# Kernel optimization log

Hardware: AMD Instinct MI355X
Metric: run time of the kernel (lower is better)

## Reference

```python
import jax, jax.numpy as jnp
import numpy as np

OBS = 256      # observation_space_size == state_vector_len
SV = 2047      # STATE_VECTORS = WMG_MAX_OBS
D = 256        # tfm_vec_size = 8 heads * 32 head_size
H = 8
HD = 32
L = 2          # TFM_NUM_LAYERS
FF = 1024      # TFM_HIDDEN_SIZE
ACH = 512      # AC_HIDDEN_LAYER_SIZE
A = 16         # action_space_size


def setup_inputs() -> dict:
    key = jax.random.key(0)
    ks = jax.random.split(key, 24)
    r = lambda k, s: (jax.random.normal(k, s, jnp.float32) * 0.02)
    inp = {
        "observation": jax.random.normal(ks[0], (OBS,), jnp.float32),
        "old_vectors": jax.random.normal(ks[1], (SV, OBS), jnp.float32),
        "W_core": r(ks[2], (OBS, D)), "b_core": jnp.zeros((D,), jnp.float32),
        # memo embedding takes cat(state_vec, age_onehot) of size OBS+SV
        "W_memo": r(ks[3], (OBS + SV, D)), "b_memo": jnp.zeros((D,), jnp.float32),
        "Wq": r(ks[4], (L, D, D)), "bq": jnp.zeros((L, D), jnp.float32),
        "Wk": r(ks[5], (L, D, D)), "bk": jnp.zeros((L, D), jnp.float32),
        "Wv": r(ks[6], (L, D, D)), "bv": jnp.zeros((L, D), jnp.float32),
        "Wo": r(ks[7], (L, D, D)), "bo": jnp.zeros((L, D), jnp.float32),
        "ln1_g": jnp.ones((L, D), jnp.float32), "ln1_b": jnp.zeros((L, D), jnp.float32),
        "ln2_g": jnp.ones((L, D), jnp.float32), "ln2_b": jnp.zeros((L, D), jnp.float32),
        "W_ff1": r(ks[8], (L, D, FF)), "b_ff1": jnp.zeros((L, FF), jnp.float32),
        "W_ff2": r(ks[9], (L, FF, D)), "b_ff2": jnp.zeros((L, D), jnp.float32),
        "aW1": r(ks[10], (D, ACH)), "ab1": jnp.zeros((ACH,), jnp.float32),
        "aW2": r(ks[11], (ACH, ACH)), "ab2": jnp.zeros((ACH,), jnp.float32),
        "aWo": r(ks[12], (ACH, A)), "abo": jnp.zeros((A,), jnp.float32),
        "cW1": r(ks[13], (D, ACH)), "cb1": jnp.zeros((ACH,), jnp.float32),
        "cW2": r(ks[14], (ACH, ACH)), "cb2": jnp.zeros((ACH,), jnp.float32),
        "cWo": r(ks[15], (ACH, 1)), "cbo": jnp.zeros((1,), jnp.float32),
    }
    return inp


def _ln(x, g, b, eps=1e-5):
    m = jnp.mean(x, axis=-1, keepdims=True)
    v = jnp.mean(jnp.square(x - m), axis=-1, keepdims=True)
    return (x - m) * jax.lax.rsqrt(v + eps) * g + b


def reference(observation, old_vectors, W_core, b_core, W_memo, b_memo,
              Wq, bq, Wk, bk, Wv, bv, Wo, bo,
              ln1_g, ln1_b, ln2_g, ln2_b, W_ff1, b_ff1, W_ff2, b_ff2,
              aW1, ab1, aW2, ab2, aWo, abo, cW1, cb1, cW2, cb2, cWo, cbo):
    # core embedding [D]
    emb0 = observation @ W_core + b_core
    # fused memo + age-onehot embedding: cat(vec_i, e_i) @ W_memo == vec_i @ W_memo[:OBS] + W_memo[OBS+i]
    memo_emb = old_vectors @ W_memo[:OBS] + W_memo[OBS:] + b_memo  # [SV, D]
    x = jnp.concatenate([emb0[None, :], memo_emb], axis=0)[None]   # [1, 1+SV, D]
    S = 1 + SV
    scale = 1.0 / np.sqrt(HD).astype(np.float32)
    for l in range(L):
        q = (x @ Wq[l] + bq[l]).reshape(1, S, H, HD)
        k = (x @ Wk[l] + bk[l]).reshape(1, S, H, HD)
        v = (x @ Wv[l] + bv[l]).reshape(1, S, H, HD)
        scores = jnp.einsum('bqhd,bkhd->bhqk', q, k) * scale       # [1,H,S,S]
        probs = jax.nn.softmax(scores, axis=-1)
        ctx = jnp.einsum('bhqk,bkhd->bqhd', probs, v).reshape(1, S, D)
        x = _ln(x + ctx @ Wo[l] + bo[l], ln1_g[l], ln1_b[l])
        h = jax.nn.gelu(x @ W_ff1[l] + b_ff1[l])
        x = _ln(x + h @ W_ff2[l] + b_ff2[l], ln2_g[l], ln2_b[l])
    t = x[:, 0, :]                                                 # [1, D]
    ha = jnp.tanh(jnp.tanh(t @ aW1 + ab1) @ aW2 + ab2)
    policy = ha @ aWo + abo                                        # [1, A] logits
    hc = jnp.tanh(jnp.tanh(t @ cW1 + cb1) @ cW2 + cb2)
    value_est = hc @ cWo + cbo                                     # [1, 1]
    # WMG_MAX_MEMOS == 0 path: new state vector is tanh(observation)
    new_vector = jnp.tanh(observation)                             # [OBS]
    return value_est, policy, new_vector
```

## Files before the change

### kernel.cpp

```cpp
#include <hip/hip_runtime.h>
#include <stdint.h>

typedef __attribute__((ext_vector_type(8))) short bf16x8;
typedef __attribute__((ext_vector_type(4))) float f32x4;

constexpr int kSEQ = 2048;
constexpr int kD   = 256;
constexpr int kHD  = 32;
constexpr int kFF  = 1024;
constexpr int kA   = 16;

__device__ __forceinline__ unsigned short f2b(float f) {
  union { float f; unsigned int u; } v; v.f = f;
  unsigned int r = v.u + 0x7FFFu + ((v.u >> 16) & 1u);
  return (unsigned short)(r >> 16);
}

struct ConvTable {
  const float* src[13];
  int K[13];
  int N[13];
  int dst[13];
  int tstart[14];
};

union SharedU {
  struct { unsigned short lt[64][72]; } cv;
  struct { unsigned short Al[64][40]; unsigned short Bl[32][40]; } g64;
  struct { unsigned short Kl[64][40]; unsigned short Vt[32][72];
           unsigned short Pl[4][16][72]; } at;
};

struct MegaParams {
  ConvTable tab;
  const float *obs, *oldv, *Wcore, *bcore, *Wmemo0, *bmemo, *Wmemo2;
  const float *bq, *bk, *bv, *bo, *ln1g, *ln1b, *ln2g, *ln2b, *bff1, *bff2;
  const float *aW1, *ab1, *aW2, *ab2, *aWo, *abo;
  const float *cW1, *cb1, *cW2, *cb2, *cWo, *cbo;
  float* xf; unsigned short* xb;
  unsigned short *qb, *kb, *vb, *wT;
  float *pacc, *pml, *h1, *h2, *out;
  int oQKV[2], oWoT[2], oFF1[2], oFF2[2];
  int convJobs, nsplit, tpb;
};

__device__ void conv_job(const MegaParams& p, SharedU& sh, int job) {
  const int tid = threadIdx.x;
  if (job == p.convJobs) {
    float a = p.bcore[tid];
    #pragma unroll 8
    for (int k = 0; k < 256; k++) a += p.obs[k] * p.Wcore[k * kD + tid];
    p.xf[tid] = a;
    p.xb[tid] = f2b(a);
    return;
  }
  int m = 0;
  while (job >= p.tab.tstart[m + 1]) m++;
  const int tloc = job - p.tab.tstart[m];
  const int N = p.tab.N[m], K = p.tab.K[m];
  const int ntile = N >> 6;
  const int k0 = (tloc / ntile) * 64, n0 = (tloc % ntile) * 64;
  const float* src = p.tab.src[m];
  {
    const int r = tid >> 2, c16 = (tid & 3) * 16;
    const float* sp = src + (size_t)(k0 + r) * N + n0 + c16;
    #pragma unroll
    for (int j = 0; j < 16; j++) sh.cv.lt[r][c16 + j] = f2b(sp[j]);
  }
  __syncthreads();
  {
    const int n = tid >> 2, kc = (tid & 3) * 16;
    unsigned short* dp = p.wT + p.tab.dst[m] + (size_t)(n0 + n) * K + k0 + kc;
    unsigned short g[16];
    #pragma unroll
    for (int j = 0; j < 16; j++) g[j] = sh.cv.lt[kc + j][n];
    *(bf16x8*)dp = *(bf16x8*)&g[0];
    *(bf16x8*)(dp + 8) = *(bf16x8*)&g[8];
  }
}

__device__ void memo_job(const MegaParams& p, SharedU& sh, int job) {
  const int tid = threadIdx.x;
  const int w = tid >> 6, l = tid & 63, lg = l >> 4, lr = l & 15;
  const int sr = tid >> 2, sk = (tid & 3) * 8;
  const int kr = tid >> 3, nc = (tid & 7) * 4;
  const int m0 = (job & 31) * 64, n0 = (job >> 5) * 32;
  f32x4 acc[2];
  #pragma unroll
  for (int c = 0; c < 2; c++)
    #pragma unroll
    for (int i = 0; i < 4; i++) acc[c][i] = 0.f;

  auto loadA = [&](int k0) -> bf16x8 {
    bf16x8 av;
    if (m0 + sr < 2047) {
      const float* ap = p.oldv + (size_t)(m0 + sr) * 256 + k0 + sk;
      #pragma unroll
      for (int j = 0; j < 8; j++) av[j] = (short)f2b(ap[j]);
    } else {
      #pragma unroll
      for (int j = 0; j < 8; j++) av[j] = 0;
    }
    return av;
  };
  auto loadB = [&](int k0, float* b4) {
    const float* bp = p.Wmemo0 + (size_t)(k0 + kr) * kD + n0 + nc;
    #pragma unroll
    for (int j = 0; j < 4; j++) b4[j] = bp[j];
  };

  bf16x8 av = loadA(0);
  float b4[4];
  loadB(0, b4);

  for (int k0 = 0; k0 < 256; k0 += 32) {
    __syncthreads();
    *(bf16x8*)&sh.g64.Al[sr][sk] = av;
    #pragma unroll
    for (int j = 0; j < 4; j++) sh.g64.Bl[nc + j][kr] = f2b(b4[j]);
    __syncthreads();
    if (k0 + 32 < 256) {
      av = loadA(k0 + 32);
      loadB(k0 + 32, b4);
    }
    bf16x8 af = *(bf16x8*)&sh.g64.Al[w * 16 + lr][8 * lg];
    #pragma unroll
    for (int c = 0; c < 2; c++) {
      bf16x8 bf = *(bf16x8*)&sh.g64.Bl[c * 16 + lr][8 * lg];
      acc[c] = __builtin_amdgcn_mfma_f32_16x16x32_bf16(af, bf, acc[c], 0, 0, 0);
    }
  }

  #pragma unroll
  for (int c = 0; c < 2; c++)
    #pragma unroll
    for (int i = 0; i < 4; i++) {
      const int gr = m0 + w * 16 + 4 * lg + i;
      const int gc = n0 + c * 16 + lr;
      if (gr >= 2047) continue;
      const float v = acc[c][i] + p.bmemo[gc] + p.Wmemo2[(size_t)gr * kD + gc];
      p.xf[(size_t)(gr + 1) * kD + gc] = v;
      p.xb[(size_t)(gr + 1) * kD + gc] = f2b(v);
    }
}

__global__ __launch_bounds__(256) void k_cvm(MegaParams p) {
  __shared__ SharedU sh;
  if (blockIdx.x < 256) memo_job(p, sh, blockIdx.x);
  else conv_job(p, sh, blockIdx.x - 256);
}

__global__ __launch_bounds__(256) void k_qkv(MegaParams p, int lyr) {
  __shared__ SharedU sh;
  const int tid = threadIdx.x;
  const int w = tid >> 6, l = tid & 63, lg = l >> 4, lr = l & 15;
  const int sr = tid >> 2, sk = (tid & 3) * 8;
  const int job = blockIdx.x;
  const int m0 = (job & 31) * 64, n0 = (job >> 5) * 32;
  const unsigned short* BT = p.wT + p.oQKV[lyr];
  f32x4 acc[2];
  #pragma unroll
  for (int c = 0; c < 2; c++)
    #pragma unroll
    for (int i = 0; i < 4; i++) acc[c][i] = 0.f;

  bf16x8 av = *(const bf16x8*)(p.xb + (size_t)(m0 + sr) * 256 + sk);
  bf16x8 bv;
  if (tid < 128) bv = *(const bf16x8*)(BT + (size_t)(n0 + sr) * 256 + sk);

  for (int k0 = 0; k0 < 256; k0 += 32) {
    __syncthreads();
    *(bf16x8*)&sh.g64.Al[sr][sk] = av;
    if (tid < 128) *(bf16x8*)&sh.g64.Bl[sr][sk] = bv;
    __syncthreads();
    if (k0 + 32 < 256) {
      av = *(const bf16x8*)(p.xb + (size_t)(m0 + sr) * 256 + k0 + 32 + sk);
      if (tid < 128)
        bv = *(const bf16x8*)(BT + (size_t)(n0 + sr) * 256 + k0 + 32 + sk);
    }
    bf16x8 af = *(bf16x8*)&sh.g64.Al[w * 16 + lr][8 * lg];
    #pragma unroll
    for (int c = 0; c < 2; c++) {
      bf16x8 bf = *(bf16x8*)&sh.g64.Bl[c * 16 + lr][8 * lg];
      acc[c] = __builtin_amdgcn_mfma_f32_16x16x32_bf16(af, bf, acc[c], 0, 0, 0);
    }
  }

  #pragma unroll
  for (int c = 0; c < 2; c++)
    #pragma unroll
    for (int i = 0; i < 4; i++) {
      const int gr = m0 + w * 16 + 4 * lg + i;
      const int gc = n0 + c * 16 + lr;
      const int t = gc >> 8, cc = gc & 255;
      const float* bp = (t == 0) ? (p.bq + lyr * 256)
                        : (t == 1 ? (p.bk + lyr * 256) : (p.bv + lyr * 256));
      unsigned short* op = (t == 0) ? p.qb : (t == 1 ? p.kb : p.vb);
      float v = acc[c][i] + bp[cc];
      if (t == 0) v *= 0.17677669529663687f;
      op[(size_t)gr * kD + cc] = f2b(v);
    }
}

__device__ void attn_job(SharedU& sh, int qb_, int h, int s, int tpb,
                         const unsigned short* q, const unsigned short* k,
                         const unsigned short* v, float* pacc, float* pml) {
  const int tid = threadIdx.x;
  const int w = tid >> 6, l = tid & 63, lg = l >> 4, lr = l & 15;
  const int q0 = qb_ * 64;
  const int hoff = h * kHD;
  const int sr = tid >> 2, sk = (tid & 3) * 8;
  const int t0 = s * tpb;

  const bf16x8 qf =
      *(const bf16x8*)(q + (size_t)(q0 + w * 16 + lr) * kD + hoff + 8 * lg);

  float m_[4], l_[4];
  f32x4 acc[2];
  #pragma unroll
  for (int i = 0; i < 4; i++) { m_[i] = -1e30f; l_[i] = 0.f; }
  #pragma unroll
  for (int dt = 0; dt < 2; dt++)
    #pragma unroll
    for (int i = 0; i < 4; i++) acc[dt][i] = 0.f;

  bf16x8 kreg = *(const bf16x8*)(k + (size_t)(t0 * 64 + sr) * kD + hoff + sk);
  bf16x8 vreg = *(const bf16x8*)(v + (size_t)(t0 * 64 + sr) * kD + hoff + sk);

  for (int t = 0; t < tpb; t++) {
    __syncthreads();
    *(bf16x8*)&sh.at.Kl[sr][sk] = kreg;
    #pragma unroll
    for (int j = 0; j < 8; j++) sh.at.Vt[sk + j][sr] = (unsigned short)vreg[j];
    __syncthreads();
    if (t + 1 < tpb) {
      const size_t nx = (size_t)((t0 + t + 1) * 64 + sr) * kD + hoff + sk;
      kreg = *(const bf16x8*)(k + nx);
      vreg = *(const bf16x8*)(v + nx);
    }
    f32x4 sc[4];
    #pragma unroll
    for (int c = 0; c < 4; c++) {
      f32x4 z;
      #pragma unroll
      for (int i = 0; i < 4; i++) z[i] = 0.f;
      bf16x8 kf = *(bf16x8*)&sh.at.Kl[c * 16 + lr][8 * lg];
      sc[c] = __builtin_amdgcn_mfma_f32_16x16x32_bf16(qf, kf, z, 0, 0, 0);
    }
    float tm[4];
    #pragma unroll
    for (int i = 0; i < 4; i++)
      tm[i] = fmaxf(fmaxf(sc[0][i], sc[1][i]), fmaxf(sc[2][i], sc[3][i]));
    #pragma unroll
    for (int mm = 1; mm <= 8; mm <<= 1)
      #pragma unroll
      for (int i = 0; i < 4; i++) tm[i] = fmaxf(tm[i], __shfl_xor(tm[i], mm));
    float pv[4][4], rs[4], corr[4];
    #pragma unroll
    for (int i = 0; i < 4; i++) {
      const float nm = fmaxf(m_[i], tm[i]);
      corr[i] = __expf(m_[i] - nm);
      m_[i] = nm;
      rs[i] = 0.f;
    }
    #pragma unroll
    for (int c = 0; c < 4; c++)
      #pragma unroll
      for (int i = 0; i < 4; i++) {
        pv[c][i] = __expf(sc[c][i] - m_[i]);
        rs[i] += pv[c][i];
      }
    #pragma unroll
    for (int mm = 1; mm <= 8; mm <<= 1)
      #pragma unroll
      for (int i = 0; i < 4; i++) rs[i] += __shfl_xor(rs[i], mm);
    #pragma unroll
    for (int i = 0; i < 4; i++) {
      l_[i] = l_[i] * corr[i] + rs[i];
      acc[0][i] *= corr[i];
      acc[1][i] *= corr[i];
    }
    #pragma unroll
    for (int c = 0; c < 4; c++)
      #pragma unroll
      for (int i = 0; i < 4; i++)
        sh.at.Pl[w][4 * lg + i][c * 16 + lr] = f2b(pv[c][i]);
    __syncthreads();
    #pragma unroll
    for (int k2 = 0; k2 < 2; k2++) {
      bf16x8 pf_ = *(bf16x8*)&sh.at.Pl[w][lr][k2 * 32 + 8 * lg];
      #pragma unroll
      for (int dt = 0; dt < 2; dt++) {
        bf16x8 vf = *(bf16x8*)&sh.at.Vt[dt * 16 + lr][k2 * 32 + 8 * lg];
        acc[dt] = __builtin_amdgcn_mfma_f32_16x16x32_bf16(pf_, vf, acc[dt], 0, 0, 0);
      }
    }
  }

  const int pb = s * 8 + h;
  float* pa = pacc + (size_t)pb * kSEQ * kHD;
  float* pm = pml + (size_t)pb * kSEQ * 2;
  #pragma unroll
  for (int dt = 0; dt < 2; dt++)
    #pragma unroll
    for (int i = 0; i < 4; i++) {
      const int gr = q0 + w * 16 + 4 * lg + i;
      pa[(size_t)gr * kHD + dt * 16 + lr] = acc[dt][i];
    }
  if (lr == 0) {
    #pragma unroll
    for (int i = 0; i < 4; i++) {
      const int gr = q0 + w * 16 + 4 * lg + i;
      float2 ml; ml.x = m_[i]; ml.y = l_[i];
      *(float2*)&pm[(size_t)gr * 2] = ml;
    }
  }
}

__global__ __launch_bounds__(256) void k_attn(MegaParams p) {
  __shared__ SharedU sh;
  const int job = blockIdx.x;
  const int qb_ = job & 31, h = (job >> 5) & 7, s = job >> 8;
  attn_job(sh, qb_, h, s, p.tpb, p.qb, p.kb, p.vb, p.pacc, p.pml);
}

__device__ __forceinline__ void ln16(float v[4][4], float2 (*red)[16],
                                     const float* gam, const float* bet,
                                     int w, int lg, int lr) {
  float ps[4], ps2[4];
  #pragma unroll
  for (int i = 0; i < 4; i++) {
    ps[i] = 0.f; ps2[i] = 0.f;
    #pragma unroll
    for (int c = 0; c < 4; c++) {
      ps[i] += v[c][i];
      ps2[i] += v[c][i] * v[c][i];
    }
  }
  #pragma unroll
  for (int mm = 1; mm <= 8; mm <<= 1)
    #pragma unroll
    for (int i = 0; i < 4; i++) {
      ps[i] += __shfl_xor(ps[i], mm);
      ps2[i] += __shfl_xor(ps2[i], mm);
    }
  if (lr == 0) {
    #pragma unroll
    for (int i = 0; i < 4; i++) {
      float2 t; t.x = ps[i]; t.y = ps2[i];
      red[w][4 * lg + i] = t;
    }
  }
  __syncthreads();
  #pragma unroll
  for (int i = 0; i < 4; i++) {
    const int ri = 4 * lg + i;
    float sx = 0.f, sx2 = 0.f;
    #pragma unroll
    for (int ww = 0; ww < 4; ww++) {
      float2 t = red[ww][ri];
      sx += t.x; sx2 += t.y;
    }
    const float mean = sx * (1.0f / 256.0f);
    const float var = sx2 * (1.0f / 256.0f) - mean * mean;
    const float rstd = rsqrtf(var + 1e-5f);
    #pragma unroll
    for (int c = 0; c < 4; c++) {
      const int col = w * 64 + c * 16 + lr;
      v[c][i] = (v[c][i] - mean) * rstd * gam[col] + bet[col];
    }
  }
}

template <bool QKV>
__global__ __launch_bounds__(256) void k_block(MegaParams p, int lyr) {
  __shared__ unsigned short As[16][264];
  __shared__ unsigned short Hs[16][1032];
  __shared__ float2 red[4][16];
  const int tid = threadIdx.x;
  const int w = tid >> 6, l = tid & 63, lg = l >> 4, lr = l & 15;
  const int r0 = blockIdx.x * 16;

  {
    const int row = r0 + (tid >> 4);
    const int kc = (tid & 15) * 16;
    const int h_ = kc >> 5;
    const int d0 = kc & 31;
    float mx = -1e30f;
    for (int s2 = 0; s2 < p.nsplit; s2++)
      mx = fmaxf(mx, p.pml[((size_t)(s2 * 8 + h_) * kSEQ + row) * 2]);
    float L = 0.f;
    float o[16];
    #pragma unroll
    for (int j = 0; j < 16; j++) o[j] = 0.f;
    for (int s2 = 0; s2 < p.nsplit; s2++) {
      const size_t pb = (size_t)(s2 * 8 + h_) * kSEQ + row;
      const float2 t = *(const float2*)&p.pml[pb * 2];
      const float es = __expf(t.x - mx);
      L += t.y * es;
      const float* pa = p.pacc + pb * kHD + d0;
      #pragma unroll
      for (int j = 0; j < 16; j++) o[j] += pa[j] * es;
    }
    const float inv = 1.0f / L;
    unsigned short* dst = &As[tid >> 4][kc];
    #pragma unroll
    for (int j = 0; j < 16; j++) dst[j] = f2b(o[j] * inv);
  }
  __syncthreads();

  float yv[4][4];
  {
    const unsigned short* BT = p.wT + p.oWoT[lyr];
    const float* bias = p.bo + lyr * kD;
    f32x4 acc[4];
    #pragma unroll
    for (int c = 0; c < 4; c++)
      #pragma unroll
      for (int i = 0; i < 4; i++) acc[c][i] = 0.f;
    #pragma unroll 2
    for (int k0 = 0; k0 < 256; k0 += 32) {
      bf16x8 af = *(bf16x8*)&As[lr][k0 + 8 * lg];
      #pragma unroll
      for (int c = 0; c < 4; c++) {
        bf16x8 bf = *(const bf16x8*)(BT + (size_t)(w * 64 + c * 16 + lr) * 256 +
                                     k0 + 8 * lg);
        acc[c] = __builtin_amdgcn_mfma_f32_16x16x32_bf16(af, bf, acc[c], 0, 0, 0);
      }
    }
    #pragma unroll
    for (int c = 0; c < 4; c++)
      #pragma unroll
      for (int i = 0; i < 4; i++) {
        const int col = w * 64 + c * 16 + lr;
        const int gr = r0 + 4 * lg + i;
        yv[c][i] = acc[c][i] + bias[col] + p.xf[(size_t)gr * kD + col];
      }
    ln16(yv, red, p.ln1g + lyr * kD, p.ln1b + lyr * kD, w, lg, lr);
    #pragma unroll
    for (int c = 0; c < 4; c++)
      #pragma unroll
      for (int i = 0; i < 4; i++)
        As[4 * lg + i][w * 64 + c * 16 + lr] = f2b(yv[c][i]);
  }
  __syncthreads();

  {
    const unsigned short* BT = p.wT + p.oFF1[lyr];
    const float* bias = p.bff1 + lyr * kFF;
    #pragma unroll 2
    for (int ct = 0; ct < 16; ct++) {
      f32x4 acc;
      #pragma unroll
      for (int i = 0; i < 4; i++) acc[i] = 0.f;
      #pragma unroll
      for (int k0 = 0; k0 < 256; k0 += 32) {
        bf16x8 af = *(bf16x8*)&As[lr][k0 + 8 * lg];
        bf16x8 bf = *(const bf16x8*)(
            BT + (size_t)(w * 256 + ct * 16 + lr) * 256 + k0 + 8 * lg);
        acc = __builtin_amdgcn_mfma_f32_16x16x32_bf16(af, bf, acc, 0, 0, 0);
      }
      const int col = w * 256 + ct * 16 + lr;
      #pragma unroll
      for (int i = 0; i < 4; i++) {
        const float v = acc[i] + bias[col];
        const float g =
            0.5f * v *
            (1.0f + tanhf(0.7978845608028654f * (v + 0.044715f * v * v * v)));
        Hs[4 * lg + i][col] = f2b(g);
      }
    }
  }
  __syncthreads();

  float zv[4][4];
  {
    const unsigned short* BT = p.wT + p.oFF2[lyr];
    const float* bias = p.bff2 + lyr * kD;
    f32x4 acc[4];
    #pragma unroll
    for (int c = 0; c < 4; c++)
      #pragma unroll
      for (int i = 0; i < 4; i++) acc[c][i] = 0.f;
    #pragma unroll 2
    for (int k0 = 0; k0 < 1024; k0 += 32) {
      bf16x8 af = *(bf16x8*)&Hs[lr][k0 + 8 * lg];
      #pragma unroll
      for (int c = 0; c < 4; c++) {
        bf16x8 bf = *(const bf16x8*)(
            BT + (size_t)(w * 64 + c * 16 + lr) * 1024 + k0 + 8 * lg);
        acc[c] = __builtin_amdgcn_mfma_f32_16x16x32_bf16(af, bf, acc[c], 0, 0, 0);
      }
    }
    #pragma unroll
    for (int c = 0; c < 4; c++)
      #pragma unroll
      for (int i = 0; i < 4; i++) {
        const int col = w * 64 + c * 16 + lr;
        zv[c][i] = acc[c][i] + bias[col] + yv[c][i];
      }
    ln16(zv, red, p.ln2g + lyr * kD, p.ln2b + lyr * kD, w, lg, lr);
    #pragma unroll
    for (int c = 0; c < 4; c++)
      #pragma unroll
      for (int i = 0; i < 4; i++) {
        const int col = w * 64 + c * 16 + lr;
        const int gr = r0 + 4 * lg + i;
        p.xf[(size_t)gr * kD + col] = zv[c][i];
        p.xb[(size_t)gr * kD + col] = f2b(zv[c][i]);
        if constexpr (QKV) As[4 * lg + i][col] = f2b(zv[c][i]);
      }
  }

  if constexpr (QKV) {
    __syncthreads();
    const unsigned short* BT = p.wT + p.oQKV[lyr + 1];
    const float* bq_ = p.bq + (lyr + 1) * 256;
    const float* bk_ = p.bk + (lyr + 1) * 256;
    const float* bv_ = p.bv + (lyr + 1) * 256;
    #pragma unroll 2
    for (int t = 0; t < 12; t++) {
      f32x4 acc;
      #pragma unroll
      for (int i = 0; i < 4; i++) acc[i] = 0.f;
      #pragma unroll
      for (int k0 = 0; k0 < 256; k0 += 32) {
        bf16x8 af = *(bf16x8*)&As[lr][k0 + 8 * lg];
        bf16x8 bf = *(const bf16x8*)(
            BT + (size_t)(w * 192 + t * 16 + lr) * 256 + k0 + 8 * lg);
        acc = __builtin_amdgcn_mfma_f32_16x16x32_bf16(af, bf, acc, 0, 0, 0);
      }
      const int gc = w * 192 + t * 16 + lr;
      const int tb = gc >> 8, cc = gc & 255;
      const float* bp = (tb == 0) ? bq_ : (tb == 1 ? bk_ : bv_);
      unsigned short* op = (tb == 0) ? p.qb : (tb == 1 ? p.kb : p.vb);
      #pragma unroll
      for (int i = 0; i < 4; i++) {
        const int gr = r0 + 4 * lg + i;
        float v = acc[i] + bp[cc];
        if (tb == 0) v *= 0.17677669529663687f;
        op[(size_t)gr * kD + cc] = f2b(v);
      }
    }
  }
}

__global__ __launch_bounds__(256) void k_h1(MegaParams p) {
  __shared__ float tl[256];
  __shared__ float red[4][64];
  const int tid = threadIdx.x;
  tl[tid] = p.xf[tid];
  __syncthreads();
  const int jj = blockIdx.x * 64;
  const bool actor = jj < 512;
  const float* W = actor ? p.aW1 : p.cW1;
  const float* b = actor ? p.ab1 : p.cb1;
  const int j0 = actor ? jj : jj - 512;
  const int ks = tid >> 6, j = tid & 63;
  float s = 0.f;
  #pragma unroll 4
  for (int k2 = ks * 64; k2 < ks * 64 + 64; k2++)
    s += tl[k2] * W[(size_t)k2 * 512 + j0 + j];
  red[ks][j] = s;
  __syncthreads();
  if (tid < 64) {
    float t = red[0][tid] + red[1][tid] + red[2][tid] + red[3][tid] + b[j0 + tid];
    p.h1[jj + tid] = tanhf(t);
  }
}

__global__ __launch_bounds__(256) void k_h2(MegaParams p) {
  __shared__ float tl[512];
  __shared__ float red[4][64];
  const int tid = threadIdx.x;
  const int jj = blockIdx.x * 64;
  const bool actor = jj < 512;
  const float* hin = actor ? p.h1 : p.h1 + 512;
  tl[tid] = hin[tid];
  tl[tid + 256] = hin[tid + 256];
  __syncthreads();
  const float* W = actor ? p.aW2 : p.cW2;
  const float* b = actor ? p.ab2 : p.cb2;
  const int j0 = actor ? jj : jj - 512;
  const int ks = tid >> 6, j = tid & 63;
  float s = 0.f;
  #pragma unroll 4
  for (int k2 = ks * 128; k2 < ks * 128 + 128; k2++)
    s += tl[k2] * W[(size_t)k2 * 512 + j0 + j];
  red[ks][j] = s;
  __syncthreads();
  if (tid < 64) {
    float t = red[0][tid] + red[1][tid] + red[2][tid] + red[3][tid] + b[j0 + tid];
    p.h2[jj + tid] = tanhf(t);
  }
}

__global__ __launch_bounds__(256) void k_h3(MegaParams p) {
  __shared__ float ha[512], hc[512], vred[4];
  const int tid = threadIdx.x;
  ha[tid] = p.h2[tid];
  ha[tid + 256] = p.h2[tid + 256];
  hc[tid] = p.h2[512 + tid];
  hc[tid + 256] = p.h2[768 + tid];
  __syncthreads();
  const int g = tid >> 4, l16 = tid & 15;
  float s = 0.f;
  for (int k2 = l16 * 32; k2 < l16 * 32 + 32; k2++)
    s += ha[k2] * p.aWo[(size_t)k2 * kA + g];
  #pragma unroll
  for (int mm = 1; mm <= 8; mm <<= 1) s += __shfl_xor(s, mm);
  if (l16 == 0) p.out[1 + g] = s + p.abo[g];
  float vv = hc[tid] * p.cWo[tid] + hc[tid + 256] * p.cWo[tid + 256];
  #pragma unroll
  for (int mm = 1; mm <= 32; mm <<= 1) vv += __shfl_xor(vv, mm);
  if ((tid & 63) == 0) vred[tid >> 6] = vv;
  __syncthreads();
  if (tid == 0)
    p.out[0] = vred[0] + vred[1] + vred[2] + vred[3] + p.cbo[0];
  p.out[17 + tid] = tanhf(p.obs[tid]);
}

extern "C" void kernel_launch(void* const* d_in, const int* in_sizes, int n_in,
                              void* d_out, int out_size, void* d_ws, size_t ws_size,
                              hipStream_t stream) {
  const float* obs   = (const float*)d_in[0];
  const float* oldv  = (const float*)d_in[1];
  const float* Wcore = (const float*)d_in[2];
  const float* bcore = (const float*)d_in[3];
  const float* Wmemo = (const float*)d_in[4];
  const float* bmemo = (const float*)d_in[5];
  const float* Wq    = (const float*)d_in[6];
  const float* bq    = (const float*)d_in[7];
  const float* Wk    = (const float*)d_in[8];
  const float* bk    = (const float*)d_in[9];
  const float* Wv    = (const float*)d_in[10];
  const float* bv    = (const float*)d_in[11];
  const float* Wo    = (const float*)d_in[12];
  const float* bo    = (const float*)d_in[13];
  const float* ln1g  = (const float*)d_in[14];
  const float* ln1b  = (const float*)d_in[15];
  const float* ln2g  = (const float*)d_in[16];
  const float* ln2b  = (const float*)d_in[17];
  const float* Wff1  = (const float*)d_in[18];
  const float* bff1  = (const float*)d_in[19];
  const float* Wff2  = (const float*)d_in[20];
  const float* bff2  = (const float*)d_in[21];

  MegaParams P;
  P.obs = obs; P.oldv = oldv; P.Wcore = Wcore; P.bcore = bcore;
  P.Wmemo0 = Wmemo; P.bmemo = bmemo; P.Wmemo2 = Wmemo + 256 * 256;
  P.bq = bq; P.bk = bk; P.bv = bv; P.bo = bo;
  P.ln1g = ln1g; P.ln1b = ln1b; P.ln2g = ln2g; P.ln2b = ln2b;
  P.bff1 = bff1; P.bff2 = bff2;
  P.aW1 = (const float*)d_in[22]; P.ab1 = (const float*)d_in[23];
  P.aW2 = (const float*)d_in[24]; P.ab2 = (const float*)d_in[25];
  P.aWo = (const float*)d_in[26]; P.abo = (const float*)d_in[27];
  P.cW1 = (const float*)d_in[28]; P.cb1 = (const float*)d_in[29];
  P.cW2 = (const float*)d_in[30]; P.cb2 = (const float*)d_in[31];
  P.cWo = (const float*)d_in[32]; P.cbo = (const float*)d_in[33];

  char* ws = (char*)d_ws;
  P.xf = (float*)(ws + 0);
  P.xb = (unsigned short*)(ws + (2u << 20));
  P.qb = (unsigned short*)(ws + (3u << 20));
  P.kb = (unsigned short*)(ws + (4u << 20));
  P.vb = (unsigned short*)(ws + (5u << 20));
  P.wT = (unsigned short*)(ws + (6u << 20));
  P.h1 = (float*)(ws + (10u << 20));
  P.h2 = (float*)(ws + (10u << 20) + 8192);
  P.out = (float*)d_out;

  int nsplit = 8;
  const size_t paccOff = (size_t)14u << 20;
  const size_t pmlOff  = (size_t)31u << 20;
  while (nsplit > 1 &&
         (paccOff + (size_t)nsplit * 8 * kSEQ * kHD * 4 > pmlOff ||
          pmlOff + (size_t)nsplit * 8 * kSEQ * 2 * 4 > ws_size))
    nsplit >>= 1;
  P.pacc = (float*)(ws + paccOff);
  P.pml  = (float*)(ws + pmlOff);
  P.nsplit = nsplit;
  P.tpb = 32 / nsplit;

  int cur = 0;
  for (int l2 = 0; l2 < 2; l2++) {
    P.oQKV[l2] = cur; cur += 196608;
    P.oWoT[l2] = cur; cur += 65536;
    P.oFF1[l2] = cur; cur += 262144;
    P.oFF2[l2] = cur; cur += 262144;
  }

  int idx = 0, ts = 0;
  auto add = [&](const float* s, int K, int N, int dst) {
    P.tab.src[idx] = s; P.tab.K[idx] = K; P.tab.N[idx] = N;
    P.tab.dst[idx] = dst; P.tab.tstart[idx] = ts;
    ts += (K >> 6) * (N >> 6); idx++;
  };
  for (int l2 = 0; l2 < 2; l2++) {
    add(Wq + l2 * 65536, 256, 256, P.oQKV[l2]);
    add(Wk + l2 * 65536, 256, 256, P.oQKV[l2] + 65536);
    add(Wv + l2 * 65536, 256, 256, P.oQKV[l2] + 131072);
    add(Wo + l2 * 65536, 256, 256, P.oWoT[l2]);
    add(Wff1 + l2 * 262144, 256, 1024, P.oFF1[l2]);
    add(Wff2 + l2 * 262144, 1024, 256, P.oFF2[l2]);
  }
  P.tab.tstart[idx] = ts;
  P.convJobs = ts;

  k_cvm<<<256 + ts + 1, 256, 0, stream>>>(P);
  k_qkv<<<768, 256, 0, stream>>>(P, 0);
  k_attn<<<256 * nsplit, 256, 0, stream>>>(P);
  k_block<true><<<128, 256, 0, stream>>>(P, 0);
  k_attn<<<256 * nsplit, 256, 0, stream>>>(P);
  k_block<false><<<128, 256, 0, stream>>>(P, 1);
  k_h1<<<16, 256, 0, stream>>>(P);
  k_h2<<<16, 256, 0, stream>>>(P);
  k_h3<<<1, 256, 0, stream>>>(P);
}
```

Measured before the change: 217.3 us.

## Widen k_block to 1024 threads with one 16-column tile per wave

Each k_block workgroup now runs 16 waves instead of 4, and each wave computes a single 16-column MFMA tile for Wo and FF2, a quarter of the FF1 and QKV columns, and a 4-element slice of the attention-combine step. With only 128 blocks launched, this is meant to put more waves on the GPU and shorten each block's serial MFMA chain. The cost is a 16-way LayerNorm reduction across waves, an extra barrier, and less reuse of each A-fragment load, since every wave reloads it from LDS for fewer MFMAs.

```diff
diff --git a/kernel.cpp b/kernel.cpp
--- a/kernel.cpp
+++ b/kernel.cpp
@@ -324,19 +324,12 @@
   attn_job(sh, qb_, h, s, p.tpb, p.qb, p.kb, p.vb, p.pacc, p.pml);
 }
 
-__device__ __forceinline__ void ln16(float v[4][4], float2 (*red)[16],
-                                     const float* gam, const float* bet,
-                                     int w, int lg, int lr) {
+__device__ __forceinline__ void ln16w(float v[4], float2 (*red)[16],
+                                      const float* gam, const float* bet,
+                                      int ww, int lg, int lr) {
   float ps[4], ps2[4];
   #pragma unroll
-  for (int i = 0; i < 4; i++) {
-    ps[i] = 0.f; ps2[i] = 0.f;
-    #pragma unroll
-    for (int c = 0; c < 4; c++) {
-      ps[i] += v[c][i];
-      ps2[i] += v[c][i] * v[c][i];
-    }
-  }
+  for (int i = 0; i < 4; i++) { ps[i] = v[i]; ps2[i] = v[i] * v[i]; }
   #pragma unroll
   for (int mm = 1; mm <= 8; mm <<= 1)
     #pragma unroll
@@ -348,7 +341,7 @@
     #pragma unroll
     for (int i = 0; i < 4; i++) {
       float2 t; t.x = ps[i]; t.y = ps2[i];
-      red[w][4 * lg + i] = t;
+      red[ww][4 * lg + i] = t;
     }
   }
   __syncthreads();
@@ -357,42 +350,39 @@
     const int ri = 4 * lg + i;
     float sx = 0.f, sx2 = 0.f;
     #pragma unroll
-    for (int ww = 0; ww < 4; ww++) {
-      float2 t = red[ww][ri];
+    for (int w2 = 0; w2 < 16; w2++) {
+      float2 t = red[w2][ri];
       sx += t.x; sx2 += t.y;
     }
     const float mean = sx * (1.0f / 256.0f);
     const float var = sx2 * (1.0f / 256.0f) - mean * mean;
     const float rstd = rsqrtf(var + 1e-5f);
-    #pragma unroll
-    for (int c = 0; c < 4; c++) {
-      const int col = w * 64 + c * 16 + lr;
-      v[c][i] = (v[c][i] - mean) * rstd * gam[col] + bet[col];
-    }
+    const int col = ww * 16 + lr;
+    v[i] = (v[i] - mean) * rstd * gam[col] + bet[col];
   }
 }
 
 template <bool QKV>
-__global__ __launch_bounds__(256) void k_block(MegaParams p, int lyr) {
+__global__ __launch_bounds__(1024) void k_block(MegaParams p, int lyr) {
   __shared__ unsigned short As[16][264];
   __shared__ unsigned short Hs[16][1032];
-  __shared__ float2 red[4][16];
-  const int tid = threadIdx.x;
-  const int w = tid >> 6, l = tid & 63, lg = l >> 4, lr = l & 15;
+  __shared__ float2 red[16][16];
+  const int tid = threadIdx.x;
+  const int ww = tid >> 6, l = tid & 63, lg = l >> 4, lr = l & 15;
   const int r0 = blockIdx.x * 16;
 
   {
-    const int row = r0 + (tid >> 4);
-    const int kc = (tid & 15) * 16;
+    const int row = r0 + (tid >> 6);
+    const int kc = (tid & 63) * 4;
     const int h_ = kc >> 5;
     const int d0 = kc & 31;
     float mx = -1e30f;
     for (int s2 = 0; s2 < p.nsplit; s2++)
       mx = fmaxf(mx, p.pml[((size_t)(s2 * 8 + h_) * kSEQ + row) * 2]);
     float L = 0.f;
-    float o[16];
-    #pragma unroll
-    for (int j = 0; j < 16; j++) o[j] = 0.f;
+    float o[4];
+    #pragma unroll
+    for (int j = 0; j < 4; j++) o[j] = 0.f;
     for (int s2 = 0; s2 < p.nsplit; s2++) {
       const size_t pb = (size_t)(s2 * 8 + h_) * kSEQ + row;
       const float2 t = *(const float2*)&p.pml[pb * 2];
@@ -400,56 +390,47 @@
       L += t.y * es;
       const float* pa = p.pacc + pb * kHD + d0;
       #pragma unroll
-      for (int j = 0; j < 16; j++) o[j] += pa[j] * es;
+      for (int j = 0; j < 4; j++) o[j] += pa[j] * es;
     }
     const float inv = 1.0f / L;
-    unsigned short* dst = &As[tid >> 4][kc];
-    #pragma unroll
-    for (int j = 0; j < 16; j++) dst[j] = f2b(o[j] * inv);
-  }
-  __syncthreads();
-
-  float yv[4][4];
+    unsigned short* dst = &As[tid >> 6][kc];
+    #pragma unroll
+    for (int j = 0; j < 4; j++) dst[j] = f2b(o[j] * inv);
+  }
+  __syncthreads();
+
+  float yv[4];
   {
     const unsigned short* BT = p.wT + p.oWoT[lyr];
     const float* bias = p.bo + lyr * kD;
-    f32x4 acc[4];
-    #pragma unroll
-    for (int c = 0; c < 4; c++)
-      #pragma unroll
-      for (int i = 0; i < 4; i++) acc[c][i] = 0.f;
-    #pragma unroll 2
+    f32x4 acc;
+    #pragma unroll
+    for (int i = 0; i < 4; i++) acc[i] = 0.f;
+    #pragma unroll
     for (int k0 = 0; k0 < 256; k0 += 32) {
       bf16x8 af = *(bf16x8*)&As[lr][k0 + 8 * lg];
-      #pragma unroll
-      for (int c = 0; c < 4; c++) {
-        bf16x8 bf = *(const bf16x8*)(BT + (size_t)(w * 64 + c * 16 + lr) * 256 +
-                                     k0 + 8 * lg);
-        acc[c] = __builtin_amdgcn_mfma_f32_16x16x32_bf16(af, bf, acc[c], 0, 0, 0);
-      }
-    }
-    #pragma unroll
-    for (int c = 0; c < 4; c++)
-      #pragma unroll
-      for (int i = 0; i < 4; i++) {
-        const int col = w * 64 + c * 16 + lr;
-        const int gr = r0 + 4 * lg + i;
-        yv[c][i] = acc[c][i] + bias[col] + p.xf[(size_t)gr * kD + col];
-      }
-    ln16(yv, red, p.ln1g + lyr * kD, p.ln1b + lyr * kD, w, lg, lr);
-    #pragma unroll
-    for (int c = 0; c < 4; c++)
-      #pragma unroll
-      for (int i = 0; i < 4; i++)
-        As[4 * lg + i][w * 64 + c * 16 + lr] = f2b(yv[c][i]);
+      bf16x8 bf = *(const bf16x8*)(BT + (size_t)(ww * 16 + lr) * 256 + k0 + 8 * lg);
+      acc = __builtin_amdgcn_mfma_f32_16x16x32_bf16(af, bf, acc, 0, 0, 0);
+    }
+    const int col = ww * 16 + lr;
+    #pragma unroll
+    for (int i = 0; i < 4; i++) {
+      const int gr = r0 + 4 * lg + i;
+      yv[i] = acc[i] + bias[col] + p.xf[(size_t)gr * kD + col];
+    }
+    ln16w(yv, red, p.ln1g + lyr * kD, p.ln1b + lyr * kD, ww, lg, lr);
+    __syncthreads();
+    #pragma unroll
+    for (int i = 0; i < 4; i++)
+      As[4 * lg + i][col] = f2b(yv[i]);
   }
   __syncthreads();
 
   {
     const unsigned short* BT = p.wT + p.oFF1[lyr];
     const float* bias = p.bff1 + lyr * kFF;
-    #pragma unroll 2
-    for (int ct = 0; ct < 16; ct++) {
+    #pragma unroll
+    for (int ct = 0; ct < 4; ct++) {
       f32x4 acc;
       #pragma unroll
       for (int i = 0; i < 4; i++) acc[i] = 0.f;
@@ -457,10 +438,10 @@
       for (int k0 = 0; k0 < 256; k0 += 32) {
         bf16x8 af = *(bf16x8*)&As[lr][k0 + 8 * lg];
         bf16x8 bf = *(const bf16x8*)(
-            BT + (size_t)(w * 256 + ct * 16 + lr) * 256 + k0 + 8 * lg);
+            BT + (size_t)(ww * 64 + ct * 16 + lr) * 256 + k0 + 8 * lg);
         acc = __builtin_amdgcn_mfma_f32_16x16x32_bf16(af, bf, acc, 0, 0, 0);
       }
-      const int col = w * 256 + ct * 16 + lr;
+      const int col = ww * 64 + ct * 16 + lr;
       #pragma unroll
       for (int i = 0; i < 4; i++) {
         const float v = acc[i] + bias[col];
@@ -473,43 +454,30 @@
   }
   __syncthreads();
 
-  float zv[4][4];
+  float zv[4];
   {
     const unsigned short* BT = p.wT + p.oFF2[lyr];
     const float* bias = p.bff2 + lyr * kD;
-    f32x4 acc[4];
-    #pragma unroll
-    for (int c = 0; c < 4; c++)
-      #pragma unroll
-      for (int i = 0; i < 4; i++) acc[c][i] = 0.f;
-    #pragma unroll 2
+    f32x4 acc;
+    #pragma unroll
+    for (int i = 0; i < 4; i++) acc[i] = 0.f;
+    #pragma unroll 8
     for (int k0 = 0; k0 < 1024; k0 += 32) {
       bf16x8 af = *(bf16x8*)&Hs[lr][k0 + 8 * lg];
-      #pragma unroll
-      for (int c = 0; c < 4; c++) {
-        bf16x8 bf = *(const bf16x8*)(
-            BT + (size_t)(w * 64 + c * 16 + lr) * 1024 + k0 + 8 * lg);
-        acc[c] = __builtin_amdgcn_mfma_f32_16x16x32_bf16(af, bf, acc[c], 0, 0, 0);
-      }
-    }
-    #pragma unroll
-    for (int c = 0; c < 4; c++)
-      #pragma unroll
-      for (int i = 0; i < 4; i++) {
-        const int col = w * 64 + c * 16 + lr;
-        zv[c][i] = acc[c][i] + bias[col] + yv[c][i];
-      }
-    ln16(zv, red, p.ln2g + lyr * kD, p.ln2b + lyr * kD, w, lg, lr);
-    #pragma unroll
-    for (int c = 0; c < 4; c++)
-      #pragma unroll
-      for (int i = 0; i < 4; i++) {
-        const int col = w * 64 + c * 16 + lr;
-        const int gr = r0 + 4 * lg + i;
-        p.xf[(size_t)gr * kD + col] = zv[c][i];
-        p.xb[(size_t)gr * kD + col] = f2b(zv[c][i]);
-        if constexpr (QKV) As[4 * lg + i][col] = f2b(zv[c][i]);
-      }
+      bf16x8 bf = *(const bf16x8*)(BT + (size_t)(ww * 16 + lr) * 1024 + k0 + 8 * lg);
+      acc = __builtin_amdgcn_mfma_f32_16x16x32_bf16(af, bf, acc, 0, 0, 0);
+    }
+    const int col = ww * 16 + lr;
+    #pragma unroll
+    for (int i = 0; i < 4; i++) zv[i] = acc[i] + bias[col] + yv[i];
+    ln16w(zv, red, p.ln2g + lyr * kD, p.ln2b + lyr * kD, ww, lg, lr);
+    #pragma unroll
+    for (int i = 0; i < 4; i++) {
+      const int gr = r0 + 4 * lg + i;
+      p.xf[(size_t)gr * kD + col] = zv[i];
+      p.xb[(size_t)gr * kD + col] = f2b(zv[i]);
+      if constexpr (QKV) As[4 * lg + i][col] = f2b(zv[i]);
+    }
   }
 
   if constexpr (QKV) {
@@ -518,8 +486,8 @@
     const float* bq_ = p.bq + (lyr + 1) * 256;
     const float* bk_ = p.bk + (lyr + 1) * 256;
     const float* bv_ = p.bv + (lyr + 1) * 256;
-    #pragma unroll 2
-    for (int t = 0; t < 12; t++) {
+    #pragma unroll
+    for (int t = 0; t < 3; t++) {
       f32x4 acc;
       #pragma unroll
       for (int i = 0; i < 4; i++) acc[i] = 0.f;
@@ -527,10 +495,10 @@
       for (int k0 = 0; k0 < 256; k0 += 32) {
         bf16x8 af = *(bf16x8*)&As[lr][k0 + 8 * lg];
         bf16x8 bf = *(const bf16x8*)(
-            BT + (size_t)(w * 192 + t * 16 + lr) * 256 + k0 + 8 * lg);
+            BT + (size_t)(ww * 48 + t * 16 + lr) * 256 + k0 + 8 * lg);
         acc = __builtin_amdgcn_mfma_f32_16x16x32_bf16(af, bf, acc, 0, 0, 0);
       }
-      const int gc = w * 192 + t * 16 + lr;
+      const int gc = ww * 48 + t * 16 + lr;
       const int tb = gc >> 8, cc = gc & 255;
       const float* bp = (tb == 0) ? bq_ : (tb == 1 ? bk_ : bv_);
       unsigned short* op = (tb == 0) ? p.qb : (tb == 1 ? p.kb : p.vb);
@@ -710,9 +678,9 @@
   k_cvm<<<256 + ts + 1, 256, 0, stream>>>(P);
   k_qkv<<<768, 256, 0, stream>>>(P, 0);
   k_attn<<<256 * nsplit, 256, 0, stream>>>(P);
-  k_block<true><<<128, 256, 0, stream>>>(P, 0);
+  k_block<true><<<128, 1024, 0, stream>>>(P, 0);
   k_attn<<<256 * nsplit, 256, 0, stream>>>(P);
-  k_block<false><<<128, 256, 0, stream>>>(P, 1);
+  k_block<false><<<128, 1024, 0, stream>>>(P, 1);
   k_h1<<<16, 256, 0, stream>>>(P);
   k_h2<<<16, 256, 0, stream>>>(P);
   k_h3<<<1, 256, 0, stream>>>(P);
```

Result: faster. 205.6 us (-5.4%).
